# Kernel optimization log

Measured on AMD Instinct MI355X. Metric: run time of the kernel, lower is better.

The kernel has to match this reference:

```python
import jax, jax.numpy as jnp
import numpy as np

KERNEL_SIZE = 25  # moving-average window (matches init kernel_size)


def setup_inputs() -> dict:
    key = jax.random.key(0)
    ks = jax.random.split(key, 5)
    B, T, N, D, O = 128, 336, 325, 3, 96
    return {
        "x": jax.random.normal(ks[0], (B, T, N, D), dtype=jnp.float32),
        "W_season": jax.random.normal(ks[1], (N, T, O), dtype=jnp.float32) * 0.02,
        "b_season": jax.random.normal(ks[2], (N, O), dtype=jnp.float32) * 0.02,
        "W_trend": jax.random.normal(ks[3], (N, T, O), dtype=jnp.float32) * 0.02,
        "b_trend": jax.random.normal(ks[4], (N, O), dtype=jnp.float32) * 0.02,
    }


def _moving_avg(z, k):
    # z: (M, T); replicate-pad (k-1)//2 at both ends, then mean over window k, stride 1.
    p = (k - 1) // 2
    xp = jnp.pad(z, ((0, 0), (p, p)), mode="edge")
    cs = jnp.concatenate(
        [jnp.zeros((z.shape[0], 1), z.dtype), jnp.cumsum(xp, axis=1)], axis=1
    )
    return (cs[:, k:] - cs[:, :-k]) / k  # (M, T) for odd k


def reference(x, W_season, b_season, W_trend, b_trend):
    B, T, N, D = x.shape
    O = W_season.shape[-1]
    # (B,T,N,D) -> (B,N,D,T) -> flat (B*N*D, T)
    z = x.transpose(0, 2, 3, 1).reshape(B * N * D, T)
    mean = _moving_avg(z, KERNEL_SIZE)
    res = z - mean
    BD = B * D
    # Faithful to the original slicing res[B*n*D : B*(n+1)*D]: contiguous blocks
    # of B*D rows per node -> reshape to (N, B*D, T).
    res_n = res.reshape(N, BD, T)
    mean_n = mean.reshape(N, BD, T)
    out_res = jnp.einsum("nbt,nto->nbo", res_n, W_season) + b_season[:, None, :]
    out_mean = jnp.einsum("nbt,nto->nbo", mean_n, W_trend) + b_trend[:, None, :]
    out = (out_res + out_mean).transpose(1, 0, 2)  # stack dim=1 -> (B*D, N, O)
    # torch .view(B, N, D, O) on contiguous (B*D, N, O), then permute(0,3,1,2)
    out = out.reshape(B, N, D, O).transpose(0, 3, 1, 2)  # (B, O, N, D)
    return out
```

## Files before the change

kernel.cpp:

```cpp
#include <hip/hip_runtime.h>
#include <hip/hip_bf16.h>

typedef __attribute__((ext_vector_type(8))) short short8;
typedef __attribute__((ext_vector_type(4))) float f32x4;

#define T_DIM   336
#define N_NODES 325
#define O_DIM   96
#define BD      384
#define ND      975
#define XB      327600
#define KT      48
#define NSTEP   7
#define MT      128
#define HALO    12
#define ZW      72
#define AST     104
#define BST     104

__device__ __forceinline__ unsigned short f2bf(float f) {
    union { __hip_bfloat16 h; unsigned short u; } cv;
    cv.h = __float2bfloat16(f);
    return cv.u;
}
__device__ __forceinline__ float bf2f(unsigned short u) {
    union { unsigned short u; __hip_bfloat16 h; } cv;
    cv.u = u;
    return __bfloat162float(cv.h);
}

__global__ __launch_bounds__(512, 4)
void dlinear_gemm(const float* __restrict__ x,
                  const float* __restrict__ Ws,
                  const float* __restrict__ bs,
                  const float* __restrict__ Wt,
                  const float* __restrict__ bt,
                  float* __restrict__ Cws)
{
    __shared__ unsigned short zext[ZW][MT];
    __shared__ unsigned short Atile[MT][AST];
    __shared__ unsigned short Btile[O_DIM][BST];
    __shared__ float biasLds[O_DIM];

    const int tid  = threadIdx.x;
    const int bid  = blockIdx.x;
    const int nn   = bid / 3;
    const int m0   = (bid % 3) * MT;
    const int r_base = nn * BD + m0;

    if (tid < O_DIM) biasLds[tid] = bs[nn*O_DIM + tid] + bt[nn*O_DIM + tid];

    const int rl   = tid & (MT-1);
    const int jb   = tid >> 7;
    const int r    = r_base + rl;
    const int bI   = r / ND;
    const int rem  = r - bI*ND;
    const float* xp = x + bI*XB + rem;

    const float* Wsn = Ws + nn*(T_DIM*O_DIM);
    const float* Wtn = Wt + nn*(T_DIM*O_DIM);

    const int wave = tid >> 6;
    const int lane = tid & 63;
    const int wm = wave & 3;
    const int wn = wave >> 2;
    const int a_row0 = wm*32 + (lane & 15);
    const int a_row1 = a_row0 + 16;
    const int b_col0 = wn*48 + (lane & 15);
    const int ksub = (lane >> 4) * 8;

    f32x4 acc[2][3];
    #pragma unroll
    for (int i = 0; i < 2; ++i)
        #pragma unroll
        for (int j = 0; j < 3; ++j)
            acc[i][j] = (f32x4){0.f, 0.f, 0.f, 0.f};

    const int tr0 = jb * 12;

    for (int s = 0; s < NSTEP; ++s) {
        const int t0 = s * KT;
        __syncthreads();

        #pragma unroll
        for (int i = 0; i < 18; ++i) {
            int j = jb + 4*i;
            int tg = t0 - HALO + j;
            tg = tg < 0 ? 0 : (tg > T_DIM-1 ? T_DIM-1 : tg);
            zext[j][rl] = f2bf(xp[tg * ND]);
        }
        #pragma unroll
        for (int i = 0; i < 9; ++i) {
            int idx = tid + i*512;
            int tr = idx / O_DIM;
            int o  = idx - tr*O_DIM;
            int go = (t0 + tr)*O_DIM + o;
            float wsv = Wsn[go];
            float wtv = Wtn[go];
            Btile[o][tr]      = f2bf(wsv);
            Btile[o][KT + tr] = f2bf(wtv - wsv);
        }
        __syncthreads();

        {
            const int row = rl;
            float S = 0.f;
            #pragma unroll
            for (int j = 0; j < 25; ++j) S += bf2f(zext[tr0 + j][row]);
            unsigned int* arow = reinterpret_cast<unsigned int*>(&Atile[row][0]);
            #pragma unroll
            for (int u = 0; u < 12; u += 2) {
                int t = tr0 + u;
                unsigned int z0 = zext[t + HALO][row];
                unsigned int z1 = zext[t + HALO + 1][row];
                arow[t >> 1] = (z1 << 16) | z0;
                unsigned short mA = f2bf(S * (1.f/25.f));
                S += bf2f(zext[t + 25][row]) - bf2f(zext[t][row]);
                unsigned short mB = f2bf(S * (1.f/25.f));
                if (u + 2 < 12)
                    S += bf2f(zext[t + 26][row]) - bf2f(zext[t + 1][row]);
                arow[(KT + t) >> 1] = ((unsigned int)mB << 16) | mA;
            }
        }
        __syncthreads();

        #pragma unroll
        for (int kc = 0; kc < 3; ++kc) {
            const int k = kc*32 + ksub;
            short8 a0 = *(const short8*)&Atile[a_row0][k];
            short8 a1 = *(const short8*)&Atile[a_row1][k];
            short8 b0 = *(const short8*)&Btile[b_col0     ][k];
            short8 b1 = *(const short8*)&Btile[b_col0 + 16][k];
            short8 b2 = *(const short8*)&Btile[b_col0 + 32][k];
            acc[0][0] = __builtin_amdgcn_mfma_f32_16x16x32_bf16(a0, b0, acc[0][0], 0, 0, 0);
            acc[1][0] = __builtin_amdgcn_mfma_f32_16x16x32_bf16(a1, b0, acc[1][0], 0, 0, 0);
            acc[0][1] = __builtin_amdgcn_mfma_f32_16x16x32_bf16(a0, b1, acc[0][1], 0, 0, 0);
            acc[1][1] = __builtin_amdgcn_mfma_f32_16x16x32_bf16(a1, b1, acc[1][1], 0, 0, 0);
            acc[0][2] = __builtin_amdgcn_mfma_f32_16x16x32_bf16(a0, b2, acc[0][2], 0, 0, 0);
            acc[1][2] = __builtin_amdgcn_mfma_f32_16x16x32_bf16(a1, b2, acc[1][2], 0, 0, 0);
        }
    }

    float* Cbase = Cws + (long)r_base * O_DIM;
    const int rsub = (lane >> 4) * 4;
    #pragma unroll
    for (int fm = 0; fm < 2; ++fm) {
        #pragma unroll
        for (int fn = 0; fn < 3; ++fn) {
            const int col = b_col0 + fn*16;
            const float bv = biasLds[col];
            #pragma unroll
            for (int j = 0; j < 4; ++j) {
                const int rowm = wm*32 + fm*16 + rsub + j;
                Cbase[rowm*O_DIM + col] = acc[fm][fn][j] + bv;
            }
        }
    }
}

__global__ __launch_bounds__(256)
void dlinear_out(const float* __restrict__ Cws, float* __restrict__ out)
{
    __shared__ float tile[65][97];
    const int m   = blockIdx.x;
    const int nn0 = blockIdx.y * 65;
    const int tid = threadIdx.x;

    for (int idx = tid; idx < 65*O_DIM; idx += 256) {
        int nni = idx / O_DIM;
        int o   = idx - nni*O_DIM;
        tile[nni][o] = Cws[(long)((nn0 + nni)*BD + m)*O_DIM + o];
    }
    __syncthreads();
    const int b = m / 3;
    const int g = m - b*3;
    float* obase = out + b*93600 + g*N_NODES + nn0;
    for (int idx = tid; idx < 65*O_DIM; idx += 256) {
        int o   = idx / 65;
        int nni = idx - o*65;
        obase[o*ND + nni] = tile[nni][o];
    }
}

extern "C" void kernel_launch(void* const* d_in, const int* in_sizes, int n_in,
                              void* d_out, int out_size, void* d_ws, size_t ws_size,
                              hipStream_t stream)
{
    const float* x  = (const float*)d_in[0];
    const float* Ws = (const float*)d_in[1];
    const float* bs = (const float*)d_in[2];
    const float* Wt = (const float*)d_in[3];
    const float* bt = (const float*)d_in[4];
    float* out = (float*)d_out;
    float* Cws = (float*)d_ws;

    dlinear_gemm<<<dim3(975), dim3(512), 0, stream>>>(x, Ws, bs, Wt, bt, Cws);
    dlinear_out<<<dim3(384, 5), dim3(256), 0, stream>>>(Cws, out);
}
```

Measured before the change: 111.5 us.

## Fold moving average into weights via prep kernel, halve GEMM K

```diff
diff --git a/kernel.cpp b/kernel.cpp
--- a/kernel.cpp
+++ b/kernel.cpp
@@ -3,6 +3,8 @@
 
 typedef __attribute__((ext_vector_type(8))) short short8;
 typedef __attribute__((ext_vector_type(4))) float f32x4;
+typedef unsigned short ushort_t;
+typedef unsigned int uint32;
 
 #define T_DIM   336
 #define N_NODES 325
@@ -10,64 +12,105 @@
 #define BD      384
 #define ND      975
 #define XB      327600
-#define KT      48
-#define NSTEP   7
+#define KT      96
+#define NSTEP   4
 #define MT      128
-#define HALO    12
-#define ZW      72
 #define AST     104
 #define BST     104
-
-__device__ __forceinline__ unsigned short f2bf(float f) {
-    union { __hip_bfloat16 h; unsigned short u; } cv;
-    cv.h = __float2bfloat16(f);
-    return cv.u;
-}
-__device__ __forceinline__ float bf2f(unsigned short u) {
-    union { unsigned short u; __hip_bfloat16 h; } cv;
-    cv.u = u;
-    return __bfloat162float(cv.h);
-}
-
-__global__ __launch_bounds__(512, 4)
+#define BSEG    10240
+#define WTO     32256
+
+static __device__ __forceinline__ uint32 pk2bf(float a, float b) {
+    union { __hip_bfloat16 h; ushort_t u; } x, y;
+    x.h = __float2bfloat16(a); y.h = __float2bfloat16(b);
+    return ((uint32)y.u << 16) | x.u;
+}
+
+static __device__ __forceinline__ void gload_lds16(const void* g, void* l) {
+    __builtin_amdgcn_global_load_lds(
+        (const __attribute__((address_space(1))) void*)g,
+        (__attribute__((address_space(3))) void*)l, 16, 0, 0);
+}
+
+__global__ __launch_bounds__(384)
+void dlinear_wprep(const float* __restrict__ Ws, const float* __restrict__ bs,
+                   const float* __restrict__ Wt, const float* __restrict__ bt,
+                   ushort_t* __restrict__ Bpack, float* __restrict__ biasArr)
+{
+    const int nn  = blockIdx.x;
+    const int tid = threadIdx.x;
+    const int o   = tid % O_DIM;
+    const int s   = tid / O_DIM;
+
+    const float* wsp = Ws + nn * WTO + o;
+    const float* wtp = Wt + nn * WTO + o;
+
+    if (s == 0) biasArr[nn*O_DIM + o] = bs[nn*O_DIM + o] + bt[nn*O_DIM + o];
+
+    const int t0 = s * KT;
+    float S = 0.f;
+    {
+        int lo = t0 - 12; if (lo < 0) lo = 0;
+        for (int t = lo; t <= t0 + 12; ++t) S += wtp[t*O_DIM] - wsp[t*O_DIM];
+    }
+
+    uint32* bp32 = (uint32*)(Bpack + (size_t)(nn*4 + s) * BSEG + o * BST);
+    float prev = 0.f;
+    #pragma unroll 1
+    for (int k = 0; k < KT; ++k) {
+        const int v = t0 + k;
+        float val = 0.f;
+        if (v < T_DIM) {
+            float Vv = S;
+            if (v == 0) {
+                Vv = 0.f;
+                for (int t = 0; t <= 12; ++t)
+                    Vv += (float)(13 - t) * (wtp[t*O_DIM] - wsp[t*O_DIM]);
+            } else if (v == T_DIM - 1) {
+                Vv = 0.f;
+                for (int t = 323; t <= 335; ++t)
+                    Vv += (float)(t - 322) * (wtp[t*O_DIM] - wsp[t*O_DIM]);
+            }
+            val = wsp[v*O_DIM] + Vv * (1.0f/25.0f);
+            if (v + 13 <= T_DIM - 1) S += wtp[(v+13)*O_DIM] - wsp[(v+13)*O_DIM];
+            if (v - 12 >= 0)         S -= wtp[(v-12)*O_DIM] - wsp[(v-12)*O_DIM];
+        }
+        if (k & 1) bp32[k >> 1] = pk2bf(prev, val); else prev = val;
+    }
+    bp32[48] = 0u; bp32[49] = 0u; bp32[50] = 0u; bp32[51] = 0u;
+}
+
+__global__ __launch_bounds__(512, 6)
 void dlinear_gemm(const float* __restrict__ x,
-                  const float* __restrict__ Ws,
-                  const float* __restrict__ bs,
-                  const float* __restrict__ Wt,
-                  const float* __restrict__ bt,
+                  const ushort_t* __restrict__ Bpack,
+                  const float* __restrict__ biasArr,
                   float* __restrict__ Cws)
 {
-    __shared__ unsigned short zext[ZW][MT];
-    __shared__ unsigned short Atile[MT][AST];
-    __shared__ unsigned short Btile[O_DIM][BST];
-    __shared__ float biasLds[O_DIM];
-
-    const int tid  = threadIdx.x;
-    const int bid  = blockIdx.x;
-    const int nn   = bid / 3;
-    const int m0   = (bid % 3) * MT;
+    __shared__ ushort_t Btile[BSEG];
+    __shared__ ushort_t Atile[MT][AST];
+
+    const int tid = threadIdx.x;
+    const int bid = blockIdx.x;
+    const int nn  = bid / 3;
+    const int m0  = (bid % 3) * MT;
     const int r_base = nn * BD + m0;
 
-    if (tid < O_DIM) biasLds[tid] = bs[nn*O_DIM + tid] + bt[nn*O_DIM + tid];
-
-    const int rl   = tid & (MT-1);
-    const int jb   = tid >> 7;
-    const int r    = r_base + rl;
-    const int bI   = r / ND;
-    const int rem  = r - bI*ND;
-    const float* xp = x + bI*XB + rem;
-
-    const float* Wsn = Ws + nn*(T_DIM*O_DIM);
-    const float* Wtn = Wt + nn*(T_DIM*O_DIM);
+    const int m   = tid & (MT-1);
+    const int tb  = (tid >> 7) * 24;
+    const int r   = r_base + m;
+    const int bI  = r / ND;
+    const int rem = r - bI * ND;
+    const float* xp = x + (size_t)bI * XB + rem;
+
+    const ushort_t* bsrc = Bpack + (size_t)nn * (4*BSEG);
 
     const int wave = tid >> 6;
     const int lane = tid & 63;
     const int wm = wave & 3;
     const int wn = wave >> 2;
     const int a_row0 = wm*32 + (lane & 15);
-    const int a_row1 = a_row0 + 16;
     const int b_col0 = wn*48 + (lane & 15);
-    const int ksub = (lane >> 4) * 8;
+    const int ksub   = (lane >> 4) * 8;
 
     f32x4 acc[2][3];
     #pragma unroll
@@ -76,62 +119,45 @@
         for (int j = 0; j < 3; ++j)
             acc[i][j] = (f32x4){0.f, 0.f, 0.f, 0.f};
 
-    const int tr0 = jb * 12;
-
     for (int s = 0; s < NSTEP; ++s) {
+        __syncthreads();
+
+        {
+            const ushort_t* bs_s = bsrc + (size_t)s * BSEG;
+            gload_lds16(bs_s + (size_t)tid*8,        &Btile[tid*8]);
+            gload_lds16(bs_s + (size_t)(tid+512)*8,  &Btile[(tid+512)*8]);
+            if (tid < 256)
+                gload_lds16(bs_s + (size_t)(tid+1024)*8, &Btile[(tid+1024)*8]);
+        }
+
         const int t0 = s * KT;
-        __syncthreads();
-
-        #pragma unroll
-        for (int i = 0; i < 18; ++i) {
-            int j = jb + 4*i;
-            int tg = t0 - HALO + j;
-            tg = tg < 0 ? 0 : (tg > T_DIM-1 ? T_DIM-1 : tg);
-            zext[j][rl] = f2bf(xp[tg * ND]);
-        }
-        #pragma unroll
-        for (int i = 0; i < 9; ++i) {
-            int idx = tid + i*512;
-            int tr = idx / O_DIM;
-            int o  = idx - tr*O_DIM;
-            int go = (t0 + tr)*O_DIM + o;
-            float wsv = Wsn[go];
-            float wtv = Wtn[go];
-            Btile[o][tr]      = f2bf(wsv);
-            Btile[o][KT + tr] = f2bf(wtv - wsv);
-        }
-        __syncthreads();
-
-        {
-            const int row = rl;
-            float S = 0.f;
+        #pragma unroll
+        for (int h = 0; h < 2; ++h) {
+            float v[12];
             #pragma unroll
-            for (int j = 0; j < 25; ++j) S += bf2f(zext[tr0 + j][row]);
-            unsigned int* arow = reinterpret_cast<unsigned int*>(&Atile[row][0]);
+            for (int u = 0; u < 12; ++u) {
+                int t  = t0 + tb + h*12 + u;
+                int tc = t < T_DIM ? t : (T_DIM-1);
+                v[u] = __builtin_nontemporal_load(&xp[tc * ND]);
+            }
+            uint32 p[6];
             #pragma unroll
-            for (int u = 0; u < 12; u += 2) {
-                int t = tr0 + u;
-                unsigned int z0 = zext[t + HALO][row];
-                unsigned int z1 = zext[t + HALO + 1][row];
-                arow[t >> 1] = (z1 << 16) | z0;
-                unsigned short mA = f2bf(S * (1.f/25.f));
-                S += bf2f(zext[t + 25][row]) - bf2f(zext[t][row]);
-                unsigned short mB = f2bf(S * (1.f/25.f));
-                if (u + 2 < 12)
-                    S += bf2f(zext[t + 26][row]) - bf2f(zext[t + 1][row]);
-                arow[(KT + t) >> 1] = ((unsigned int)mB << 16) | mA;
-            }
+            for (int u = 0; u < 6; ++u) p[u] = pk2bf(v[2*u], v[2*u+1]);
+            uint32* arow = (uint32*)&Atile[m][tb + h*12];
+            *(uint2*)&arow[0] = make_uint2(p[0], p[1]);
+            *(uint2*)&arow[2] = make_uint2(p[2], p[3]);
+            *(uint2*)&arow[4] = make_uint2(p[4], p[5]);
         }
         __syncthreads();
 
         #pragma unroll
         for (int kc = 0; kc < 3; ++kc) {
             const int k = kc*32 + ksub;
-            short8 a0 = *(const short8*)&Atile[a_row0][k];
-            short8 a1 = *(const short8*)&Atile[a_row1][k];
-            short8 b0 = *(const short8*)&Btile[b_col0     ][k];
-            short8 b1 = *(const short8*)&Btile[b_col0 + 16][k];
-            short8 b2 = *(const short8*)&Btile[b_col0 + 32][k];
+            short8 a0 = *(const short8*)&Atile[a_row0     ][k];
+            short8 a1 = *(const short8*)&Atile[a_row0 + 16][k];
+            short8 b0 = *(const short8*)&Btile[(b_col0     )*BST + k];
+            short8 b1 = *(const short8*)&Btile[(b_col0 + 16)*BST + k];
+            short8 b2 = *(const short8*)&Btile[(b_col0 + 32)*BST + k];
             acc[0][0] = __builtin_amdgcn_mfma_f32_16x16x32_bf16(a0, b0, acc[0][0], 0, 0, 0);
             acc[1][0] = __builtin_amdgcn_mfma_f32_16x16x32_bf16(a1, b0, acc[1][0], 0, 0, 0);
             acc[0][1] = __builtin_amdgcn_mfma_f32_16x16x32_bf16(a0, b1, acc[0][1], 0, 0, 0);
@@ -141,14 +167,15 @@
         }
     }
 
-    float* Cbase = Cws + (long)r_base * O_DIM;
+    float* Cbase = Cws + (size_t)r_base * O_DIM;
+    const float* bfp = biasArr + nn * O_DIM;
     const int rsub = (lane >> 4) * 4;
     #pragma unroll
     for (int fm = 0; fm < 2; ++fm) {
         #pragma unroll
         for (int fn = 0; fn < 3; ++fn) {
             const int col = b_col0 + fn*16;
-            const float bv = biasLds[col];
+            const float bv = bfp[col];
             #pragma unroll
             for (int j = 0; j < 4; ++j) {
                 const int rowm = wm*32 + fm*16 + rsub + j;
@@ -169,12 +196,12 @@
     for (int idx = tid; idx < 65*O_DIM; idx += 256) {
         int nni = idx / O_DIM;
         int o   = idx - nni*O_DIM;
-        tile[nni][o] = Cws[(long)((nn0 + nni)*BD + m)*O_DIM + o];
+        tile[nni][o] = Cws[(size_t)((nn0 + nni)*BD + m)*O_DIM + o];
     }
     __syncthreads();
     const int b = m / 3;
     const int g = m - b*3;
-    float* obase = out + b*93600 + g*N_NODES + nn0;
+    float* obase = out + (size_t)b*93600 + g*N_NODES + nn0;
     for (int idx = tid; idx < 65*O_DIM; idx += 256) {
         int o   = idx / 65;
         int nni = idx - o*65;
@@ -194,6 +221,10 @@
     float* out = (float*)d_out;
     float* Cws = (float*)d_ws;
 
-    dlinear_gemm<<<dim3(975), dim3(512), 0, stream>>>(x, Ws, bs, Wt, bt, Cws);
-    dlinear_out<<<dim3(384, 5), dim3(256), 0, stream>>>(Cws, out);
-}
+    ushort_t* Bpack  = (ushort_t*)d_out;
+    float*    biasAr = (float*)d_out + 6656000;
+
+    dlinear_wprep<<<dim3(N_NODES), dim3(384), 0, stream>>>(Ws, bs, Wt, bt, Bpack, biasAr);
+    dlinear_gemm <<<dim3(975),     dim3(512), 0, stream>>>(x, Bpack, biasAr, Cws);
+    dlinear_out  <<<dim3(384, 5),  dim3(256), 0, stream>>>(Cws, out);
+}
```

Result: slower. 185.9 us (+66.7%).
